# Performance work log

Hardware: AMD Instinct MI355X
Metric: run time of the kernel (lower is better)

The kernel has to match this reference:

```python
import jax, jax.numpy as jnp
import numpy as np

B, T, D, H = 4, 2048, 1024, 16
HD = D // H  # 64

def rotate_half(x):
    x1, x2 = x[..., :x.shape[-1] // 2], x[..., x.shape[-1] // 2:]
    return jnp.concatenate((-x2, x1), axis=-1)

def setup_inputs() -> dict:
    key = jax.random.key(0)
    ks = jax.random.split(key, 8)
    x = jax.random.normal(ks[0], (B, T, D), dtype=jnp.float32)
    # causal mask: attn position (i,j) allowed iff j <= i
    mask = jnp.tril(jnp.ones((T, T), dtype=bool))[None, None]  # (1,1,T,T)
    # RoPE tables
    inv_freq = 1.0 / (10000.0 ** (np.arange(0, HD, 2, dtype=np.float32) / HD))
    t = np.arange(T, dtype=np.float32)
    freqs = np.einsum('t,f->tf', t, inv_freq)              # (T, HD/2)
    emb = np.concatenate([freqs, freqs], axis=-1)          # (T, HD)
    cos = jnp.asarray(np.cos(emb))[None, None]             # (1,1,T,HD)
    sin = jnp.asarray(np.sin(emb))[None, None]
    s = 0.02
    Wq = jax.random.normal(ks[1], (D, D), dtype=jnp.float32) * s
    Wk = jax.random.normal(ks[2], (D, D), dtype=jnp.float32) * s
    Wv = jax.random.normal(ks[3], (D, D), dtype=jnp.float32) * s
    Wo = jax.random.normal(ks[4], (D, D), dtype=jnp.float32) * s
    bq = jnp.zeros((D,), jnp.float32); bk = jnp.zeros((D,), jnp.float32)
    bv = jnp.zeros((D,), jnp.float32); bo = jnp.zeros((D,), jnp.float32)
    return dict(x=x, mask=mask, cos=cos, sin=sin, Wq=Wq, bq=bq, Wk=Wk, bk=bk,
                Wv=Wv, bv=bv, Wo=Wo, bo=bo)

def reference(x, mask, cos, sin, Wq, bq, Wk, bk, Wv, bv, Wo, bo):
    Bx, Tx, C = x.shape
    scale = (C // H) ** -0.5
    def split(h):  # (B,T,C) -> (B,H,T,HD)
        return h.reshape(Bx, Tx, H, C // H).transpose(0, 2, 1, 3)
    q = split(x @ Wq + bq)
    k = split(x @ Wk + bk)
    v = split(x @ Wv + bv)
    q = q * cos + rotate_half(q) * sin
    k = k * cos + rotate_half(k) * sin
    attn = jnp.einsum('bhqd,bhkd->bhqk', q, k) * scale
    attn = jnp.where(mask, attn, -jnp.inf)
    attn = jax.nn.softmax(attn, axis=-1)
    out = jnp.einsum('bhqk,bhkd->bhqd', attn, v)
    out = out.transpose(0, 2, 1, 3).reshape(Bx, Tx, C)
    return out @ Wo + bo
```

## Files before the change

kernel.cpp:

```cpp
#include <hip/hip_runtime.h>
#include <math.h>

typedef unsigned short u16;
typedef unsigned int   u32;
typedef __bf16  bf16x8 __attribute__((ext_vector_type(8)));
typedef short   s16x4  __attribute__((ext_vector_type(4)));
typedef float   f32x4  __attribute__((ext_vector_type(4)));

#define B_  4
#define T_  2048
#define D_  1024
#define H_  16
#define HD_ 64
#define M_  (B_*T_)
#define NEG_BIG (-30000.0f)

__device__ __forceinline__ float bf2f(u16 h) {
    u32 u = ((u32)h) << 16;
    return __uint_as_float(u);
}
__device__ __forceinline__ u16 f2bf(float f) {
    u32 u = __float_as_uint(f);
    u32 r = (u + 0x7fffu + ((u >> 16) & 1u)) >> 16;
    return (u16)r;
}
__device__ __forceinline__ void async_copy16(const u16* g, u16* l) {
    __builtin_amdgcn_global_load_lds(
        (const __attribute__((address_space(1))) u32*)g,
        (__attribute__((address_space(3))) u32*)l, 16, 0, 0);
}

__global__ __launch_bounds__(256)
void convert_x(const float* __restrict__ X, u16* __restrict__ Xb)
{
    const int id = (blockIdx.x * 256 + threadIdx.x) * 8;
    float4 f0 = *(const float4*)(X + id);
    float4 f1 = *(const float4*)(X + id + 4);
    union { u16 t[8]; uint4 v; } c;
    c.t[0] = f2bf(f0.x); c.t[1] = f2bf(f0.y); c.t[2] = f2bf(f0.z); c.t[3] = f2bf(f0.w);
    c.t[4] = f2bf(f1.x); c.t[5] = f2bf(f1.y); c.t[6] = f2bf(f1.z); c.t[7] = f2bf(f1.w);
    *(uint4*)(Xb + id) = c.v;
}

template<int OUT_F32>
__global__ __launch_bounds__(256)
void gemm_bt(const u16* __restrict__ A, const u16* __restrict__ Bt_base,
             const float* __restrict__ bias0, const float* __restrict__ bias1,
             const float* __restrict__ bias2,
             void* __restrict__ C_base, int M, int N, int K)
{
    const int z = blockIdx.z;
    const u16* Bt  = Bt_base + (size_t)z * N * K;
    const float* bias = (z == 0) ? bias0 : ((z == 1) ? bias1 : bias2);

    const int m0 = blockIdx.x * 128, n0 = blockIdx.y * 128;
    const int tid = threadIdx.x, lane = tid & 63, wave = tid >> 6;
    const int wm = (wave >> 1) * 64, wn = (wave & 1) * 64;
    const int quad = lane >> 4, l16 = lane & 15;
    const int z3 = l16 & 7;

    __shared__ __align__(16) u16 As[128 * 64];
    __shared__ __align__(16) u16 Bs[128 * 64];

    const int c0 = 8 * (quad ^ z3);
    const int c1 = 8 * ((quad | 4) ^ z3);

    f32x4 acc[4][4];
#pragma unroll
    for (int i = 0; i < 4; i++)
#pragma unroll
        for (int j = 0; j < 4; j++) acc[i][j] = (f32x4){0.f, 0.f, 0.f, 0.f};

    for (int k0 = 0; k0 < K; k0 += 64) {
        __syncthreads();
#pragma unroll
        for (int i = 0; i < 4; i++) {
            int idx = i * 256 + tid;
            int r = idx >> 3;
            int sc = 8 * ((idx & 7) ^ (r & 7));
            async_copy16(A  + (size_t)(m0 + r) * K + k0 + sc, &As[idx * 8]);
            async_copy16(Bt + (size_t)(n0 + r) * K + k0 + sc, &Bs[idx * 8]);
        }
        __syncthreads();

#pragma unroll
        for (int ks = 0; ks < 2; ks++) {
            const int cc = ks ? c1 : c0;
            bf16x8 af[4], bfr[4];
#pragma unroll
            for (int mi = 0; mi < 4; mi++)
                af[mi] = *(const bf16x8*)&As[(wm + mi * 16 + l16) * 64 + cc];
#pragma unroll
            for (int ni = 0; ni < 4; ni++)
                bfr[ni] = *(const bf16x8*)&Bs[(wn + ni * 16 + l16) * 64 + cc];
#pragma unroll
            for (int mi = 0; mi < 4; mi++)
#pragma unroll
                for (int ni = 0; ni < 4; ni++)
                    acc[mi][ni] = __builtin_amdgcn_mfma_f32_16x16x32_bf16(
                        af[mi], bfr[ni], acc[mi][ni], 0, 0, 0);
        }
    }

    float bv[4];
#pragma unroll
    for (int ni = 0; ni < 4; ni++) bv[ni] = bias[n0 + wn + ni * 16 + l16];
#pragma unroll
    for (int mi = 0; mi < 4; mi++) {
#pragma unroll
        for (int reg = 0; reg < 4; reg++) {
            int row = m0 + wm + mi * 16 + quad * 4 + reg;
#pragma unroll
            for (int ni = 0; ni < 4; ni++) {
                int col = n0 + wn + ni * 16 + l16;
                float v = acc[mi][ni][reg] + bv[ni];
                if (OUT_F32)
                    ((float*)C_base + (size_t)z * M * N)[(size_t)row * N + col] = v;
                else
                    ((u16*)C_base + (size_t)z * M * N)[(size_t)row * N + col] = f2bf(v);
            }
        }
    }
}

__global__ __launch_bounds__(256)
void transpose_w(const float* __restrict__ w0, const float* __restrict__ w1,
                 const float* __restrict__ w2,
                 u16* __restrict__ out)
{
    const int z = blockIdx.z;
    const float* W = (z == 0) ? w0 : ((z == 1) ? w1 : w2);
    u16* Wt = out + (size_t)z * D_ * D_;
    const int k0 = blockIdx.x * 64, n0 = blockIdx.y * 64;
    __shared__ u16 tl[64][72];
    const int tid = threadIdx.x;
    const int r = tid >> 2, c4 = (tid & 3) * 16;
#pragma unroll
    for (int j = 0; j < 4; j++) {
        float4 fv = *(const float4*)(W + (size_t)(k0 + r) * D_ + n0 + c4 + j * 4);
        tl[r][c4 + j * 4 + 0] = f2bf(fv.x);
        tl[r][c4 + j * 4 + 1] = f2bf(fv.y);
        tl[r][c4 + j * 4 + 2] = f2bf(fv.z);
        tl[r][c4 + j * 4 + 3] = f2bf(fv.w);
    }
    __syncthreads();
    u16 vals[16];
#pragma unroll
    for (int j = 0; j < 16; j++) vals[j] = tl[c4 + j][r];
#pragma unroll
    for (int j = 0; j < 2; j++)
        *(uint4*)(Wt + (size_t)(n0 + r) * D_ + k0 + c4 + j * 8) =
            *(const uint4*)&vals[j * 8];
}

__global__ __launch_bounds__(256)
void transpose_v(const u16* __restrict__ V, u16* __restrict__ Vt)
{
    const int t0 = blockIdx.x * 64;
    const int h = blockIdx.y, b = blockIdx.z;
    __shared__ u16 tl[64][72];
    const int tid = threadIdx.x;
    const int r = tid >> 2, c4 = (tid & 3) * 16;
    const u16* Vg = V + ((size_t)(b * T_ + t0)) * D_ + h * HD_;
#pragma unroll
    for (int j = 0; j < 2; j++)
        *(uint4*)&tl[r][c4 + j * 8] =
            *(const uint4*)(Vg + (size_t)r * D_ + c4 + j * 8);
    __syncthreads();
    u16 vals[16];
#pragma unroll
    for (int j = 0; j < 16; j++) vals[j] = tl[c4 + j][r];
    u16* Og = Vt + ((size_t)(b * H_ + h)) * HD_ * T_ + (size_t)r * T_ + t0 + c4;
#pragma unroll
    for (int j = 0; j < 2; j++)
        *(uint4*)(Og + j * 8) = *(const uint4*)&vals[j * 8];
}

__global__ __launch_bounds__(256)
void rope_qk(u16* __restrict__ Q, u16* __restrict__ K,
             const float* __restrict__ cosb, const float* __restrict__ sinb)
{
    int g  = blockIdx.x * 256 + threadIdx.x;
    int d0 = (g & 3) * 8;
    int h  = (g >> 2) & (H_ - 1);
    int bt = g >> 6;
    int t  = bt & (T_ - 1);
    size_t off = (size_t)bt * D_ + h * HD_ + d0;

    const float* cp = cosb + (size_t)t * HD_ + d0;
    const float* sp = sinb + (size_t)t * HD_ + d0;
    float4 c1a = *(const float4*)(cp);
    float4 c1b = *(const float4*)(cp + 4);
    float4 s1a = *(const float4*)(sp);
    float4 s1b = *(const float4*)(sp + 4);
    float4 c2a = *(const float4*)(cp + 32);
    float4 c2b = *(const float4*)(cp + 36);
    float4 s2a = *(const float4*)(sp + 32);
    float4 s2b = *(const float4*)(sp + 36);
    float c1[8] = {c1a.x,c1a.y,c1a.z,c1a.w,c1b.x,c1b.y,c1b.z,c1b.w};
    float s1[8] = {s1a.x,s1a.y,s1a.z,s1a.w,s1b.x,s1b.y,s1b.z,s1b.w};
    float c2[8] = {c2a.x,c2a.y,c2a.z,c2a.w,c2b.x,c2b.y,c2b.z,c2b.w};
    float s2[8] = {s2a.x,s2a.y,s2a.z,s2a.w,s2b.x,s2b.y,s2b.z,s2b.w};

    {
        union { u16 t[8]; uint4 v; } x1, x2, o1, o2;
        x1.v = *(const uint4*)(Q + off);
        x2.v = *(const uint4*)(Q + off + 32);
#pragma unroll
        for (int j = 0; j < 8; j++) {
            float a = bf2f(x1.t[j]), b = bf2f(x2.t[j]);
            o1.t[j] = f2bf(a * c1[j] - b * s1[j]);
            o2.t[j] = f2bf(b * c2[j] + a * s2[j]);
        }
        *(uint4*)(Q + off)      = o1.v;
        *(uint4*)(Q + off + 32) = o2.v;
    }
    {
        union { u16 t[8]; uint4 v; } x1, x2, o1, o2;
        x1.v = *(const uint4*)(K + off);
        x2.v = *(const uint4*)(K + off + 32);
#pragma unroll
        for (int j = 0; j < 8; j++) {
            float a = bf2f(x1.t[j]), b = bf2f(x2.t[j]);
            o1.t[j] = f2bf(a * c1[j] - b * s1[j]);
            o2.t[j] = f2bf(b * c2[j] + a * s2[j]);
        }
        *(uint4*)(K + off)      = o1.v;
        *(uint4*)(K + off + 32) = o2.v;
    }
}

__global__ __launch_bounds__(512, 2)
void attn_kernel(const u16* __restrict__ Q, const u16* __restrict__ K,
                 const u16* __restrict__ Vt, u16* __restrict__ O)
{
    const int id = blockIdx.x;
    const int xcd = id & 7, rr = id >> 3;
    const int qb = 15 - (rr >> 3);
    const int hb = xcd + 8 * (rr & 7);
    const int h = hb & 15, b = hb >> 4;
    const int tid = threadIdx.x, lane = tid & 63, wave = tid >> 6;
    const int quad = lane >> 4, l16 = lane & 15;
    const int z3 = l16 & 7;

    __shared__ __align__(16) u16 Ks[2 * 8192];
    __shared__ __align__(16) u16 Vs[2 * 8192];

    const u16* Qr = Q + ((size_t)(b * T_ + qb * 128 + wave * 16 + l16)) * D_ + h * HD_;
    bf16x8 qf[2];
    {
        const float qscale = 0.125f * 1.44269504f;
        union { u16 t[8]; bf16x8 v; } a, c;
#pragma unroll
        for (int ks = 0; ks < 2; ks++) {
            a.v = *(const bf16x8*)(Qr + ks * 32 + quad * 8);
#pragma unroll
            for (int j = 0; j < 8; j++) c.t[j] = f2bf(bf2f(a.t[j]) * qscale);
            qf[ks] = c.v;
        }
    }

    s16x4 ones4;
    {
        union { u16 t[4]; s16x4 v; } o;
        const u16 one = (l16 == 0) ? (u16)0x3F80 : (u16)0;
#pragma unroll
        for (int j = 0; j < 4; j++) o.t[j] = one;
        ones4 = o.v;
    }

    const u16* Kbase = K + ((size_t)(b * T_)) * D_ + h * HD_;
    const u16* Vbase = Vt + ((size_t)(b * H_ + h)) * HD_ * T_;

    f32x4 o_acc[4], o_l;
#pragma unroll
    for (int i = 0; i < 4; i++) o_acc[i] = (f32x4){0.f, 0.f, 0.f, 0.f};
    o_l = (f32x4){0.f, 0.f, 0.f, 0.f};
    float m_i = NEG_BIG;

    const int kb0 = l16 * 64 + 8 * (quad ^ z3);
    const int kb1 = l16 * 64 + 8 * ((quad | 4) ^ z3);
    const int vsw = l16 << 3, vq = quad * 4;

    const int nkb = qb + 1;

#define STAGE(KB, BSEL)                                                        \
    {                                                                          \
        const u16* Kg = Kbase + (size_t)(KB) * 128 * D_;                       \
        const u16* Vg = Vbase + (size_t)(KB) * 128;                            \
        u16* Kd = &Ks[(BSEL) * 8192];                                          \
        u16* Vd = &Vs[(BSEL) * 8192];                                          \
        _Pragma("unroll")                                                      \
        for (int i_ = 0; i_ < 2; i_++) {                                       \
            int idx = i_ * 512 + tid;                                          \
                       \
            int kr = idx >> 3, kblk = idx & 7;                                 \
            async_copy16(Kg + (size_t)kr * D_ + ((kblk ^ (kr & 7)) * 8),       \
                         Kd + idx * 8);                                        \
                 \
            int dv = idx >> 4, sv = idx & 15;                                  \
            async_copy16(Vg + (size_t)dv * T_ + 8 * (sv ^ (dv & 15)),          \
                         Vd + idx * 8);                                        \
        }                                                                      \
    }

    STAGE(0, 0);
    __syncthreads();

    int cur = 0;
    for (int kb = 0; kb < nkb; kb++) {
        if (kb + 1 < nkb) STAGE(kb + 1, cur ^ 1);

        const u16* Kc = &Ks[cur * 8192];
        const u16* Vc = &Vs[cur * 8192];

        const int nLim = (kb == nkb - 1) ? (wave + 1) : 8;

        f32x4 s[8];
#pragma unroll
        for (int ni = 0; ni < 8; ni++) s[ni] = (f32x4){0.f, 0.f, 0.f, 0.f};
        __builtin_amdgcn_s_setprio(1);
#pragma unroll
        for (int ni = 0; ni < 8; ni++)
            if (ni < nLim) {
                bf16x8 b0 = *(const bf16x8*)&Kc[kb0 + ni * 1024];
                s[ni] = __builtin_amdgcn_mfma_f32_16x16x32_bf16(b0, qf[0], s[ni], 0, 0, 0);
                bf16x8 b1 = *(const bf16x8*)&Kc[kb1 + ni * 1024];
                s[ni] = __builtin_amdgcn_mfma_f32_16x16x32_bf16(b1, qf[1], s[ni], 0, 0, 0);
            }
        __builtin_amdgcn_s_setprio(0);

        if (kb == nkb - 1) {
            const int qrow = qb * 128 + wave * 16 + l16;
            const int kc0 = kb * 128 + quad * 4;
#pragma unroll
            for (int ni = 0; ni < 8; ni++)
                if (ni < nLim)
#pragma unroll
                    for (int r = 0; r < 4; r++)
                        s[ni][r] = (kc0 + ni * 16 + r <= qrow) ? s[ni][r] : NEG_BIG;
        }

        float m8[8];
#pragma unroll
        for (int ni = 0; ni < 8; ni++)
            m8[ni] = (ni < nLim)
                ? fmaxf(fmaxf(s[ni][0], s[ni][1]), fmaxf(s[ni][2], s[ni][3]))
                : NEG_BIG;
        float mnew = fmaxf(fmaxf(fmaxf(m8[0], m8[1]), fmaxf(m8[2], m8[3])),
                           fmaxf(fmaxf(m8[4], m8[5]), fmaxf(m8[6], m8[7])));
        mnew = fmaxf(mnew, __shfl_xor(mnew, 16, 64));
        mnew = fmaxf(mnew, __shfl_xor(mnew, 32, 64));

        if (!__all(mnew <= m_i)) {
            float mo = m_i;
            m_i = fmaxf(m_i, mnew);
            float alpha = __builtin_amdgcn_exp2f(mo - m_i);
            const int asrc = quad * 20;
            float a_o[4];
#pragma unroll
            for (int r = 0; r < 4; r++) a_o[r] = __shfl(alpha, asrc + r, 64);
#pragma unroll
            for (int i = 0; i < 4; i++)
#pragma unroll
                for (int r = 0; r < 4; r++) o_acc[i][r] *= a_o[r];
#pragma unroll
            for (int r = 0; r < 4; r++) o_l[r] *= a_o[r];
        }

        s16x4 pa[8];
#pragma unroll
        for (int ni = 0; ni < 8; ni++)
            if (ni < nLim) {
                union { u16 t[4]; s16x4 v; } c;
#pragma unroll
                for (int r = 0; r < 4; r++) {
                    float p = __builtin_amdgcn_exp2f(s[ni][r] - m_i);
                    union { __bf16 b; u16 u; } cv;
                    cv.b = (__bf16)p;
                    c.t[r] = cv.u;
                }
                pa[ni] = c.v;
            }

        __builtin_amdgcn_s_setprio(1);
#pragma unroll
        for (int ni = 0; ni < 8; ni++)
            if (ni < nLim) {
#pragma unroll
                for (int d0i = 0; d0i < 4; d0i++) {
                    int uidx = (d0i * 16 + l16) * 128 + ((ni * 16 + vq) ^ vsw);
                    s16x4 vb = *(const s16x4*)&Vc[uidx];
                    o_acc[d0i] = __builtin_amdgcn_mfma_f32_16x16x16bf16_1k(
                        pa[ni], vb, o_acc[d0i], 0, 0, 0);
                }
                o_l = __builtin_amdgcn_mfma_f32_16x16x16bf16_1k(
                    pa[ni], ones4, o_l, 0, 0, 0);
            }
        __builtin_amdgcn_s_setprio(0);

        __syncthreads();
        cur ^= 1;
    }

    float inv_o[4];
#pragma unroll
    for (int r = 0; r < 4; r++) {
        float lv = __shfl(o_l[r], lane & 48, 64);
        inv_o[r] = 1.f / fmaxf(lv, 1e-30f);
    }

    u16* Og = O + ((size_t)(b * T_ + qb * 128)) * D_ + h * HD_;
#pragma unroll
    for (int d0i = 0; d0i < 4; d0i++)
#pragma unroll
        for (int r = 0; r < 4; r++)
            Og[(size_t)(wave * 16 + quad * 4 + r) * D_ + d0i * 16 + l16] =
                f2bf(o_acc[d0i][r] * inv_o[r]);
#undef STAGE
}

extern "C" void kernel_launch(void* const* d_in, const int* in_sizes, int n_in,
                              void* d_out, int out_size, void* d_ws, size_t ws_size,
                              hipStream_t stream)
{
    (void)in_sizes; (void)n_in; (void)out_size; (void)ws_size;
    const float* x    = (const float*)d_in[0];
    const float* cosb = (const float*)d_in[2];
    const float* sinb = (const float*)d_in[3];
    const float* Wq   = (const float*)d_in[4];
    const float* bq   = (const float*)d_in[5];
    const float* Wk   = (const float*)d_in[6];
    const float* bk   = (const float*)d_in[7];
    const float* Wv   = (const float*)d_in[8];
    const float* bv   = (const float*)d_in[9];
    const float* Wo   = (const float*)d_in[10];
    const float* bo   = (const float*)d_in[11];

    u16* ws = (u16*)d_ws;
    const size_t MD = (size_t)M_ * D_;
    u16* xb     = (u16*)d_out;
    u16* Qbuf   = ws;
    u16* Kbuf   = ws + MD;
    u16* Vbuf   = ws + 2 * MD;
    u16* WtQKV  = ws + 3 * MD;
    u16* Vtbuf  = ws + 3 * MD;
    u16* WtO    = ws + MD;
    u16* Abuf   = ws;

    convert_x<<<dim3(M_ * D_ / 2048), 256, 0, stream>>>(x, xb);
    transpose_w<<<dim3(16, 16, 3), 256, 0, stream>>>(Wq, Wk, Wv, WtQKV);
    gemm_bt<0><<<dim3(64, 8, 3), 256, 0, stream>>>(xb, WtQKV, bq, bk, bv,
                                                   Qbuf, M_, D_, D_);
    rope_qk<<<dim3((B_ * T_ * H_ * 4) / 256), 256, 0, stream>>>(
        Qbuf, Kbuf, cosb, sinb);
    transpose_v<<<dim3(32, 16, 4), 256, 0, stream>>>(Vbuf, Vtbuf);
    attn_kernel<<<dim3(1024), 512, 0, stream>>>(Qbuf, Kbuf, Vtbuf, Abuf);
    transpose_w<<<dim3(16, 16, 1), 256, 0, stream>>>(Wo, Wo, Wo, WtO);
    gemm_bt<1><<<dim3(64, 8, 1), 256, 0, stream>>>(Abuf, WtO, bo, bo, bo,
                                                   d_out, M_, D_, D_);
}
```

Measured before the change: 286.9 us.

## Fuse RoPE and V transpose into QKV GEMM epilogue, remap blocks per XCD

The QKV GEMM epilogue now applies RoPE to Q and K using the cos/sin tables and writes V straight into the transposed per-head layout, so the separate rope_qk and transpose_v kernels are gone. This removes two launches and a full read-modify-write pass over Q, K and V. Both GEMMs also switch to a 1D grid with an XCD-aware block remapping so neighbouring M tiles share an XCD's L2. The price is a heavier epilogue with scattered 2-byte stores and per-row cos/sin loads, and V writes of 8 bytes strided by T.

```diff
diff --git a/kernel.cpp b/kernel.cpp
--- a/kernel.cpp
+++ b/kernel.cpp
@@ -42,18 +42,25 @@
     *(uint4*)(Xb + id) = c.v;
 }
 
-template<int OUT_F32>
 __global__ __launch_bounds__(256)
-void gemm_bt(const u16* __restrict__ A, const u16* __restrict__ Bt_base,
-             const float* __restrict__ bias0, const float* __restrict__ bias1,
-             const float* __restrict__ bias2,
-             void* __restrict__ C_base, int M, int N, int K)
-{
-    const int z = blockIdx.z;
-    const u16* Bt  = Bt_base + (size_t)z * N * K;
+void gemm_qkv(const u16* __restrict__ A, const u16* __restrict__ Bt_base,
+              const float* __restrict__ bias0, const float* __restrict__ bias1,
+              const float* __restrict__ bias2,
+              const float* __restrict__ cosb, const float* __restrict__ sinb,
+              u16* __restrict__ QK_base, u16* __restrict__ VtOut)
+{
+    const int id = blockIdx.x;
+    const int xcd = id & 7, rr = id >> 3;
+    const int m_blk = xcd * 8 + (rr & 7);
+    const int rest = rr >> 3;
+    const int n_blk = rest & 7;
+    const int z = rest >> 3;
+    const int m0 = m_blk * 128, n0 = n_blk * 128;
+    const int K = D_, N = D_;
+
+    const u16* Bt = Bt_base + (size_t)z * N * K;
     const float* bias = (z == 0) ? bias0 : ((z == 1) ? bias1 : bias2);
 
-    const int m0 = blockIdx.x * 128, n0 = blockIdx.y * 128;
     const int tid = threadIdx.x, lane = tid & 63, wave = tid >> 6;
     const int wm = (wave >> 1) * 64, wn = (wave & 1) * 64;
     const int quad = lane >> 4, l16 = lane & 15;
@@ -105,6 +112,112 @@
     float bv[4];
 #pragma unroll
     for (int ni = 0; ni < 4; ni++) bv[ni] = bias[n0 + wn + ni * 16 + l16];
+
+    if (z < 2) {
+        u16* Cz = QK_base + (size_t)z * M_ * N;
+#pragma unroll
+        for (int mi = 0; mi < 4; mi++) {
+#pragma unroll
+            for (int reg = 0; reg < 4; reg++) {
+                int row = m0 + wm + mi * 16 + quad * 4 + reg;
+                int t = row & (T_ - 1);
+                const float* cr = cosb + (size_t)t * HD_;
+                const float* sr = sinb + (size_t)t * HD_;
+                u16* Crow = Cz + (size_t)row * N + n0 + wn;
+#pragma unroll
+                for (int ni = 0; ni < 2; ni++) {
+                    int dd = ni * 16 + l16;
+                    float x1 = acc[mi][ni][reg] + bv[ni];
+                    float x2 = acc[mi][ni + 2][reg] + bv[ni + 2];
+                    float cc1 = cr[dd],      ss1 = sr[dd];
+                    float cc2 = cr[dd + 32], ss2 = sr[dd + 32];
+                    Crow[dd]      = f2bf(x1 * cc1 - x2 * ss1);
+                    Crow[dd + 32] = f2bf(x2 * cc2 + x1 * ss2);
+                }
+            }
+        }
+    } else {
+        const int bb = m0 >> 11;
+#pragma unroll
+        for (int mi = 0; mi < 4; mi++) {
+            int row0 = m0 + wm + mi * 16 + quad * 4;
+            int t = row0 & (T_ - 1);
+#pragma unroll
+            for (int ni = 0; ni < 4; ni++) {
+                int col = n0 + wn + ni * 16 + l16;
+                int h = col >> 6, dd = col & 63;
+                union { u16 t4[4]; uint2 v; } pk;
+#pragma unroll
+                for (int reg = 0; reg < 4; reg++)
+                    pk.t4[reg] = f2bf(acc[mi][ni][reg] + bv[ni]);
+                *(uint2*)(VtOut + ((size_t)(bb * H_ + h) * HD_ + dd) * T_ + t) = pk.v;
+            }
+        }
+    }
+}
+
+__global__ __launch_bounds__(256)
+void gemm_proj(const u16* __restrict__ A, const u16* __restrict__ Bt,
+               const float* __restrict__ bias,
+               float* __restrict__ C, int M, int N, int K)
+{
+    const int id = blockIdx.x;
+    const int xcd = id & 7, rr = id >> 3;
+    const int m_blk = xcd * 8 + (rr & 7);
+    const int n_blk = rr >> 3;
+    const int m0 = m_blk * 128, n0 = n_blk * 128;
+
+    const int tid = threadIdx.x, lane = tid & 63, wave = tid >> 6;
+    const int wm = (wave >> 1) * 64, wn = (wave & 1) * 64;
+    const int quad = lane >> 4, l16 = lane & 15;
+    const int z3 = l16 & 7;
+
+    __shared__ __align__(16) u16 As[128 * 64];
+    __shared__ __align__(16) u16 Bs[128 * 64];
+
+    const int c0 = 8 * (quad ^ z3);
+    const int c1 = 8 * ((quad | 4) ^ z3);
+
+    f32x4 acc[4][4];
+#pragma unroll
+    for (int i = 0; i < 4; i++)
+#pragma unroll
+        for (int j = 0; j < 4; j++) acc[i][j] = (f32x4){0.f, 0.f, 0.f, 0.f};
+
+    for (int k0 = 0; k0 < K; k0 += 64) {
+        __syncthreads();
+#pragma unroll
+        for (int i = 0; i < 4; i++) {
+            int idx = i * 256 + tid;
+            int r = idx >> 3;
+            int sc = 8 * ((idx & 7) ^ (r & 7));
+            async_copy16(A  + (size_t)(m0 + r) * K + k0 + sc, &As[idx * 8]);
+            async_copy16(Bt + (size_t)(n0 + r) * K + k0 + sc, &Bs[idx * 8]);
+        }
+        __syncthreads();
+
+#pragma unroll
+        for (int ks = 0; ks < 2; ks++) {
+            const int cc = ks ? c1 : c0;
+            bf16x8 af[4], bfr[4];
+#pragma unroll
+            for (int mi = 0; mi < 4; mi++)
+                af[mi] = *(const bf16x8*)&As[(wm + mi * 16 + l16) * 64 + cc];
+#pragma unroll
+            for (int ni = 0; ni < 4; ni++)
+                bfr[ni] = *(const bf16x8*)&Bs[(wn + ni * 16 + l16) * 64 + cc];
+#pragma unroll
+            for (int mi = 0; mi < 4; mi++)
+#pragma unroll
+                for (int ni = 0; ni < 4; ni++)
+                    acc[mi][ni] = __builtin_amdgcn_mfma_f32_16x16x32_bf16(
+                        af[mi], bfr[ni], acc[mi][ni], 0, 0, 0);
+        }
+    }
+
+    float bv[4];
+#pragma unroll
+    for (int ni = 0; ni < 4; ni++) bv[ni] = bias[n0 + wn + ni * 16 + l16];
 #pragma unroll
     for (int mi = 0; mi < 4; mi++) {
 #pragma unroll
@@ -113,11 +226,7 @@
 #pragma unroll
             for (int ni = 0; ni < 4; ni++) {
                 int col = n0 + wn + ni * 16 + l16;
-                float v = acc[mi][ni][reg] + bv[ni];
-                if (OUT_F32)
-                    ((float*)C_base + (size_t)z * M * N)[(size_t)row * N + col] = v;
-                else
-                    ((u16*)C_base + (size_t)z * M * N)[(size_t)row * N + col] = f2bf(v);
+                C[(size_t)row * N + col] = acc[mi][ni][reg] + bv[ni];
             }
         }
     }
@@ -151,83 +260,6 @@
     for (int j = 0; j < 2; j++)
         *(uint4*)(Wt + (size_t)(n0 + r) * D_ + k0 + c4 + j * 8) =
             *(const uint4*)&vals[j * 8];
-}
-
-__global__ __launch_bounds__(256)
-void transpose_v(const u16* __restrict__ V, u16* __restrict__ Vt)
-{
-    const int t0 = blockIdx.x * 64;
-    const int h = blockIdx.y, b = blockIdx.z;
-    __shared__ u16 tl[64][72];
-    const int tid = threadIdx.x;
-    const int r = tid >> 2, c4 = (tid & 3) * 16;
-    const u16* Vg = V + ((size_t)(b * T_ + t0)) * D_ + h * HD_;
-#pragma unroll
-    for (int j = 0; j < 2; j++)
-        *(uint4*)&tl[r][c4 + j * 8] =
-            *(const uint4*)(Vg + (size_t)r * D_ + c4 + j * 8);
-    __syncthreads();
-    u16 vals[16];
-#pragma unroll
-    for (int j = 0; j < 16; j++) vals[j] = tl[c4 + j][r];
-    u16* Og = Vt + ((size_t)(b * H_ + h)) * HD_ * T_ + (size_t)r * T_ + t0 + c4;
-#pragma unroll
-    for (int j = 0; j < 2; j++)
-        *(uint4*)(Og + j * 8) = *(const uint4*)&vals[j * 8];
-}
-
-__global__ __launch_bounds__(256)
-void rope_qk(u16* __restrict__ Q, u16* __restrict__ K,
-             const float* __restrict__ cosb, const float* __restrict__ sinb)
-{
-    int g  = blockIdx.x * 256 + threadIdx.x;
-    int d0 = (g & 3) * 8;
-    int h  = (g >> 2) & (H_ - 1);
-    int bt = g >> 6;
-    int t  = bt & (T_ - 1);
-    size_t off = (size_t)bt * D_ + h * HD_ + d0;
-
-    const float* cp = cosb + (size_t)t * HD_ + d0;
-    const float* sp = sinb + (size_t)t * HD_ + d0;
-    float4 c1a = *(const float4*)(cp);
-    float4 c1b = *(const float4*)(cp + 4);
-    float4 s1a = *(const float4*)(sp);
-    float4 s1b = *(const float4*)(sp + 4);
-    float4 c2a = *(const float4*)(cp + 32);
-    float4 c2b = *(const float4*)(cp + 36);
-    float4 s2a = *(const float4*)(sp + 32);
-    float4 s2b = *(const float4*)(sp + 36);
-    float c1[8] = {c1a.x,c1a.y,c1a.z,c1a.w,c1b.x,c1b.y,c1b.z,c1b.w};
-    float s1[8] = {s1a.x,s1a.y,s1a.z,s1a.w,s1b.x,s1b.y,s1b.z,s1b.w};
-    float c2[8] = {c2a.x,c2a.y,c2a.z,c2a.w,c2b.x,c2b.y,c2b.z,c2b.w};
-    float s2[8] = {s2a.x,s2a.y,s2a.z,s2a.w,s2b.x,s2b.y,s2b.z,s2b.w};
-
-    {
-        union { u16 t[8]; uint4 v; } x1, x2, o1, o2;
-        x1.v = *(const uint4*)(Q + off);
-        x2.v = *(const uint4*)(Q + off + 32);
-#pragma unroll
-        for (int j = 0; j < 8; j++) {
-            float a = bf2f(x1.t[j]), b = bf2f(x2.t[j]);
-            o1.t[j] = f2bf(a * c1[j] - b * s1[j]);
-            o2.t[j] = f2bf(b * c2[j] + a * s2[j]);
-        }
-        *(uint4*)(Q + off)      = o1.v;
-        *(uint4*)(Q + off + 32) = o2.v;
-    }
-    {
-        union { u16 t[8]; uint4 v; } x1, x2, o1, o2;
-        x1.v = *(const uint4*)(K + off);
-        x2.v = *(const uint4*)(K + off + 32);
-#pragma unroll
-        for (int j = 0; j < 8; j++) {
-            float a = bf2f(x1.t[j]), b = bf2f(x2.t[j]);
-            o1.t[j] = f2bf(a * c1[j] - b * s1[j]);
-            o2.t[j] = f2bf(b * c2[j] + a * s2[j]);
-        }
-        *(uint4*)(K + off)      = o1.v;
-        *(uint4*)(K + off + 32) = o2.v;
-    }
 }
 
 __global__ __launch_bounds__(512, 2)
@@ -293,11 +325,9 @@
         _Pragma("unroll")                                                      \
         for (int i_ = 0; i_ < 2; i_++) {                                       \
             int idx = i_ * 512 + tid;                                          \
-                       \
             int kr = idx >> 3, kblk = idx & 7;                                 \
             async_copy16(Kg + (size_t)kr * D_ + ((kblk ^ (kr & 7)) * 8),       \
                          Kd + idx * 8);                                        \
-                 \
             int dv = idx >> 4, sv = idx & 15;                                  \
             async_copy16(Vg + (size_t)dv * T_ + 8 * (sv ^ (dv & 15)),          \
                          Vd + idx * 8);                                        \
@@ -442,21 +472,18 @@
     u16* xb     = (u16*)d_out;
     u16* Qbuf   = ws;
     u16* Kbuf   = ws + MD;
-    u16* Vbuf   = ws + 2 * MD;
+    u16* Vtbuf  = ws + 2 * MD;
     u16* WtQKV  = ws + 3 * MD;
-    u16* Vtbuf  = ws + 3 * MD;
     u16* WtO    = ws + MD;
     u16* Abuf   = ws;
+    (void)Kbuf;
 
     convert_x<<<dim3(M_ * D_ / 2048), 256, 0, stream>>>(x, xb);
     transpose_w<<<dim3(16, 16, 3), 256, 0, stream>>>(Wq, Wk, Wv, WtQKV);
-    gemm_bt<0><<<dim3(64, 8, 3), 256, 0, stream>>>(xb, WtQKV, bq, bk, bv,
-                                                   Qbuf, M_, D_, D_);
-    rope_qk<<<dim3((B_ * T_ * H_ * 4) / 256), 256, 0, stream>>>(
-        Qbuf, Kbuf, cosb, sinb);
-    transpose_v<<<dim3(32, 16, 4), 256, 0, stream>>>(Vbuf, Vtbuf);
-    attn_kernel<<<dim3(1024), 512, 0, stream>>>(Qbuf, Kbuf, Vtbuf, Abuf);
+    gemm_qkv<<<dim3(1536), 256, 0, stream>>>(xb, WtQKV, bq, bk, bv,
+                                             cosb, sinb, Qbuf, Vtbuf);
+    attn_kernel<<<dim3(1024), 512, 0, stream>>>(Qbuf, ws + MD, Vtbuf, Abuf);
     transpose_w<<<dim3(16, 16, 1), 256, 0, stream>>>(Wo, Wo, Wo, WtO);
-    gemm_bt<1><<<dim3(64, 8, 1), 256, 0, stream>>>(Abuf, WtO, bo, bo, bo,
-                                                   d_out, M_, D_, D_);
-}
+    gemm_proj<<<dim3(512), 256, 0, stream>>>(Abuf, WtO, bo,
+                                             (float*)d_out, M_, D_, D_);
+}
```

New measurement: 283.1 us. Within noise of the previous version (-1.3%).
